# Kernel optimization log

Measured on AMD Instinct MI355X. Metric: run time of the kernel, lower is better.

The kernel has to match this reference:

```python
import jax, jax.numpy as jnp
import numpy as np

B, L = 128, 256
VOCAB, E, PF = 50000, 300, 50
C, K, R = 512, 3, 53
D3 = (E + 2 * PF) * 3  # 1200, conv input channels


def setup_inputs() -> dict:
    key = jax.random.key(0)
    ks = jax.random.split(key, 12)
    return {
        "context": jax.random.randint(ks[0], (B, L), 0, VOCAB),
        "subject_idx": jnp.sort(jax.random.randint(ks[1], (B, 2), 0, L), axis=-1),
        "object_idx": jnp.sort(jax.random.randint(ks[2], (B, 2), 0, L), axis=-1),
        "subject_dis": jax.random.randint(ks[3], (B, L), 0, 2 * L),
        "object_dis": jax.random.randint(ks[4], (B, L), 0, 2 * L),
        "embed_table": jax.random.normal(ks[5], (VOCAB, E), dtype=jnp.float32),
        "pos_table": jax.random.normal(ks[6], (2 * L, PF), dtype=jnp.float32),
        "conv_w": jax.random.normal(ks[7], (C, D3, K), dtype=jnp.float32) * (1.0 / np.sqrt(D3 * K)),
        "conv_b": jax.random.normal(ks[8], (C,), dtype=jnp.float32) * 0.01,
        "rela_linear_w": jax.random.normal(ks[9], (R, C), dtype=jnp.float32) * (1.0 / np.sqrt(C)),
        "rela_emb": jax.random.normal(ks[10], (R, C), dtype=jnp.float32),
    }


def _span_mean(wf3, idx):
    # mean of wf3[b, start:end+1, :] per sample, vectorized with a mask
    pos = jnp.arange(wf3.shape[1])[None, :]
    m = ((pos >= idx[:, 0:1]) & (pos <= idx[:, 1:2])).astype(wf3.dtype)  # B,L
    return jnp.einsum("bld,bl->bd", wf3, m) / jnp.sum(m, axis=1, keepdims=True)


def reference(context, subject_idx, object_idx, subject_dis, object_dis,
              embed_table, pos_table, conv_w, conv_b, rela_linear_w, rela_emb):
    emb = embed_table[context]                                            # B,L,E
    posf = jnp.concatenate([pos_table[subject_dis], pos_table[object_dis]], axis=2)
    wf = jnp.concatenate([emb, posf], axis=2)                             # B,L,D
    wp = jnp.pad(wf, ((0, 0), (1, 1), (0, 0)))
    # sliding window concat of [i-1, i, i+1]
    wf3 = jnp.concatenate([wp[:, :-2], wp[:, 1:-1], wp[:, 2:]], axis=2)   # B,L,3D

    subj = _span_mean(wf3, subject_idx)                                   # B,3D
    obj = _span_mean(wf3, object_idx)
    rs = jax.nn.softmax(jnp.einsum("bld,bd->bl", wf3, subj), axis=1)
    ro = jax.nn.softmax(jnp.einsum("bld,bd->bl", wf3, obj), axis=1)
    wf3 = wf3 * ((rs + ro) * 0.5)[:, :, None]

    x = jnp.transpose(wf3, (0, 2, 1))                                     # B,3D,L
    y = jax.lax.conv_general_dilated(x, conv_w, (1,), [(K // 2, K // 2)],
                                     dimension_numbers=("NCH", "OIH", "NCH"))
    sent = jnp.transpose(jnp.tanh(y + conv_b[None, :, None]), (0, 2, 1))  # B,L,C

    attn = jnp.einsum("blr,rc->blc",
                      jnp.einsum("blc,rc->blr", sent, rela_linear_w), rela_emb)
    attn = jax.nn.softmax(attn, axis=1)  # softmax over sequence positions
    wo = jnp.max(sent * attn, axis=1)                                     # B,C
    wo = wo / jnp.maximum(jnp.linalg.norm(wo, axis=1, keepdims=True), 1e-12)
    all_dist = jnp.linalg.norm(wo[:, None, :] - rela_emb[None, :, :], axis=2)  # B,R
    return all_dist
```

## Files before the change

kernel.cpp:

```cpp
#include <hip/hip_runtime.h>
#include <hip/hip_bf16.h>
#include <math.h>

#define B_  128
#define L_  256
#define E_  300
#define PF_ 50
#define D_  400
#define D3_ 1200
#define C_  512
#define KW_ 3
#define R_  53
#define M_  (B_*L_)
#define KP_ 1216
#define K3_ (3*KP_)
#define LROWS_ 258

typedef __attribute__((ext_vector_type(8))) short bf16x8;
typedef __attribute__((ext_vector_type(8))) unsigned short u16x8;
typedef __attribute__((ext_vector_type(4))) float f32x4;

__device__ __forceinline__ unsigned short f2bf(float f) {
    union { float f; unsigned u; } x; x.f = f;
    unsigned r = x.u + 0x7FFF + ((x.u >> 16) & 1);
    return (unsigned short)(r >> 16);
}
__device__ __forceinline__ float bf2f(unsigned short u) {
    union { unsigned u; float f; } x; x.u = ((unsigned)u) << 16;
    return x.f;
}

__device__ __forceinline__ void gld16(const void* g, void* l) {
    __builtin_amdgcn_global_load_lds(
        (const __attribute__((address_space(1))) void*)g,
        (__attribute__((address_space(3))) void*)l, 16, 0, 0);
}

__global__ void prep_wpT_kernel(const float* __restrict__ conv_w, unsigned short* __restrict__ WpT) {
    int idx = blockIdx.x * blockDim.x + threadIdx.x;
    if (idx >= C_ * K3_) return;
    int c = idx / K3_, q = idx % K3_;
    int k = q / KP_, ch = q % KP_;
    WpT[idx] = (ch < D3_) ? f2bf(conv_w[c * (D3_ * KW_) + ch * KW_ + k]) : (unsigned short)0;
}

__global__ void prep_mT_kernel(const float* __restrict__ rlw, const float* __restrict__ re,
                               unsigned short* __restrict__ MmatT) {
    int idx = blockIdx.x * blockDim.x + threadIdx.x;
    if (idx >= C_ * C_) return;
    int n = idx / C_, k = idx % C_;
    float acc = 0.f;
    for (int r = 0; r < R_; ++r)
        acc += rlw[r * C_ + k] * re[r * C_ + n];
    MmatT[idx] = f2bf(acc);
}

__global__ void build_wf_kernel(const int* __restrict__ ctx, const int* __restrict__ sdis,
                                const int* __restrict__ odis, const float* __restrict__ emb,
                                const float* __restrict__ pos, float* __restrict__ wf) {
    const int total = M_ * D_;
    for (int idx = blockIdx.x * blockDim.x + threadIdx.x; idx < total;
         idx += gridDim.x * blockDim.x) {
        int d = idx % D_;
        int bt = idx / D_;
        float v;
        if (d < E_)            v = emb[(long)ctx[bt] * E_ + d];
        else if (d < E_ + PF_) v = pos[sdis[bt] * PF_ + (d - E_)];
        else                   v = pos[odis[bt] * PF_ + (d - E_ - PF_)];
        wf[idx] = v;
    }
}

__global__ void prefix_wf_kernel(const float* __restrict__ wf, float* __restrict__ Pref) {
    int idx = blockIdx.x * blockDim.x + threadIdx.x;
    if (idx >= B_ * D_) return;
    int b = idx / D_, d = idx % D_;
    const float* src = wf + (size_t)(b << 8) * D_ + d;
    float* dst = Pref + (size_t)(b << 8) * D_ + d;
    float acc = 0.f;
    for (int t = 0; t < L_; ++t) {
        acc += src[(size_t)t * D_];
        dst[(size_t)t * D_] = acc;
    }
}

__global__ void span_mean_kernel(const float* __restrict__ Pref,
                                 const int* __restrict__ sidx, const int* __restrict__ oidx,
                                 float* __restrict__ SS, float* __restrict__ OS) {
    int idx = blockIdx.x * blockDim.x + threadIdx.x;
    if (idx >= B_ * 3 * D_) return;
    int b = idx / (3 * D_);
    int r = idx % (3 * D_);
    int j = r / D_, d = r % D_;

    {
        int s0 = sidx[b * 2], s1 = sidx[b * 2 + 1];
        float inv = 1.f / (float)(s1 - s0 + 1);
        int lo = s0 + j - 1, hi = s1 + j - 1;
        int loc = lo < 0 ? 0 : lo;
        int hic = hi > (L_ - 1) ? (L_ - 1) : hi;
        float sum = 0.f;
        if (loc <= hic) {
            float a = Pref[((size_t)((b << 8) + hic)) * D_ + d];
            float c = (loc > 0) ? Pref[((size_t)((b << 8) + loc - 1)) * D_ + d] : 0.f;
            sum = a - c;
        }
        SS[((size_t)(b * 3 + j)) * D_ + d] = sum * inv;
    }
    {
        int s0 = oidx[b * 2], s1 = oidx[b * 2 + 1];
        float inv = 1.f / (float)(s1 - s0 + 1);
        int lo = s0 + j - 1, hi = s1 + j - 1;
        int loc = lo < 0 ? 0 : lo;
        int hic = hi > (L_ - 1) ? (L_ - 1) : hi;
        float sum = 0.f;
        if (loc <= hic) {
            float a = Pref[((size_t)((b << 8) + hic)) * D_ + d];
            float c = (loc > 0) ? Pref[((size_t)((b << 8) + loc - 1)) * D_ + d] : 0.f;
            sum = a - c;
        }
        OS[((size_t)(b * 3 + j)) * D_ + d] = sum * inv;
    }
}

__global__ __launch_bounds__(256) void dots_kernel(
    const float* __restrict__ wf, const float* __restrict__ SS, const float* __restrict__ OS,
    float* __restrict__ dsb, float* __restrict__ ddb) {
    const int wave = threadIdx.x >> 6, lane = threadIdx.x & 63;
    const int g = blockIdx.x * 4 + wave;
    const int b = g >> 8, t = g & 255;
    float ds = 0.f, dd = 0.f;
#pragma unroll
    for (int j = 0; j < 3; ++j) {
        int u = t + j - 1;
        if ((unsigned)u < (unsigned)L_) {
            const float4* w  = (const float4*)(wf + ((size_t)((b << 8) + u)) * D_);
            const float4* ss = (const float4*)(SS + ((size_t)(b * 3 + j)) * D_);
            const float4* oo = (const float4*)(OS + ((size_t)(b * 3 + j)) * D_);
            for (int q = lane; q < D_ / 4; q += 64) {
                float4 wv = w[q], sv = ss[q], ov = oo[q];
                ds += wv.x * sv.x + wv.y * sv.y + wv.z * sv.z + wv.w * sv.w;
                dd += wv.x * ov.x + wv.y * ov.y + wv.z * ov.z + wv.w * ov.w;
            }
        }
    }
#pragma unroll
    for (int off = 32; off > 0; off >>= 1) {
        ds += __shfl_down(ds, off);
        dd += __shfl_down(dd, off);
    }
    if (lane == 0) { dsb[g] = ds; ddb[g] = dd; }
}

__global__ __launch_bounds__(256) void softmax_s_kernel(
    const float* __restrict__ dsb, const float* __restrict__ ddb, float* __restrict__ s) {
    const int b = blockIdx.x, tid = threadIdx.x;
    __shared__ float red[256];
    float ds = dsb[(b << 8) + tid];
    float dd = ddb[(b << 8) + tid];

    red[tid] = ds; __syncthreads();
    for (int st = 128; st > 0; st >>= 1) {
        if (tid < st) red[tid] = fmaxf(red[tid], red[tid + st]);
        __syncthreads();
    }
    float ms = red[0]; __syncthreads();
    float es = expf(ds - ms);
    red[tid] = es; __syncthreads();
    for (int st = 128; st > 0; st >>= 1) {
        if (tid < st) red[tid] += red[tid + st];
        __syncthreads();
    }
    float zs = red[0]; __syncthreads();

    red[tid] = dd; __syncthreads();
    for (int st = 128; st > 0; st >>= 1) {
        if (tid < st) red[tid] = fmaxf(red[tid], red[tid + st]);
        __syncthreads();
    }
    float mo = red[0]; __syncthreads();
    float eo = expf(dd - mo);
    red[tid] = eo; __syncthreads();
    for (int st = 128; st > 0; st >>= 1) {
        if (tid < st) red[tid] += red[tid + st];
        __syncthreads();
    }
    float zo = red[0];

    s[(b << 8) + tid] = 0.5f * (es / zs + eo / zo);
}

__global__ void build_xsp_kernel(const float* __restrict__ wf, const float* __restrict__ s,
                                 unsigned short* __restrict__ XSp) {
    const int CH8 = KP_ / 8;
    int idx = blockIdx.x * blockDim.x + threadIdx.x;
    const int total = B_ * LROWS_ * CH8;
    if (idx >= total) return;
    int chunk = idx % CH8;
    int rb = idx / CH8;
    int row = rb % LROWS_;
    int b = rb / LROWS_;

    u16x8 out = {0,0,0,0,0,0,0,0};
    int t = row - 1;
    int ch0 = chunk * 8;
    if ((unsigned)t < (unsigned)L_ && ch0 < D3_) {
        int j = ch0 / D_;
        int d0 = ch0 - j * D_;
        int u = t + j - 1;
        if ((unsigned)u < (unsigned)L_) {
            float sc = s[(b << 8) + t];
            const float* w = wf + ((size_t)((b << 8) + u)) * D_ + d0;
#pragma unroll
            for (int q = 0; q < 8; ++q) out[q] = f2bf(sc * w[q]);
        }
    }
    *(u16x8*)&XSp[((size_t)(b * LROWS_ + row)) * KP_ + ch0] = out;
}

template<int MODE>
__global__ __launch_bounds__(512, 2) void gemm8_kernel(
    const unsigned short* __restrict__ Aglob, const unsigned short* __restrict__ Bglob,
    const float* __restrict__ conv_b, unsigned short* __restrict__ outb,
    float* __restrict__ outf) {
    extern __shared__ unsigned short lds[];
    const int tid = threadIdx.x;
    const int lane = tid & 63;
    const int wave = tid >> 6;
    const int wr = wave >> 2;
    const int wc = wave & 3;
    const int bx = blockIdx.x;
    const int blockN = blockIdx.y * 256;
    const int l15 = lane & 15;
    const int NT = (MODE == 0) ? (K3_ / 64) : (C_ / 64);
    const size_t Astr = (MODE == 0) ? (size_t)KP_ : (size_t)C_;
    const size_t Bstr = (MODE == 0) ? (size_t)K3_ : (size_t)C_;

    const int arole = wc;
    const int bhalf = wc >> 1;
    const int brole = wr * 2 + (wc & 1);

    const int acol0 = (((lane >> 4) + 0) ^ (l15 & 7)) * 8;
    const int acol1 = (((lane >> 4) + 4) ^ (l15 & 7)) * 8;
    const int bro = (wc & 1) * 64;

    auto stageA = [&](int kt, int buf) {
        const unsigned short* gb;
        if constexpr (MODE == 0) {
            int tap = kt / KP_, ch0 = kt - tap * KP_;
            gb = Aglob + ((size_t)(bx * LROWS_ + wr * 128 + tap)) * KP_ + ch0;
        } else {
            gb = Aglob + ((size_t)(bx * 256 + wr * 128)) * C_ + kt;
        }
        unsigned short* pb = &lds[(buf * 2 + wr) * 8192];
#pragma unroll
        for (int i = 0; i < 4; ++i) {
            int sl = arole * 256 + i * 64 + lane;
            int row = sl >> 3, p = sl & 7;
            int colg = p ^ (row & 7);
            gld16(gb + (size_t)row * Astr + colg * 8, (char*)pb + sl * 16);
        }
    };
    auto stageB = [&](int kt, int buf) {
        const unsigned short* gb = Bglob + ((size_t)(blockN + bhalf * 128)) * Bstr + kt;
        unsigned short* pb = &lds[32768 + (buf * 2 + bhalf) * 8192];
#pragma unroll
        for (int i = 0; i < 4; ++i) {
            int sl = brole * 256 + i * 64 + lane;
            int row = sl >> 3, p = sl & 7;
            int colg = p ^ (row & 7);
            gld16(gb + (size_t)row * Bstr + colg * 8, (char*)pb + sl * 16);
        }
    };

    f32x4 acc[8][4] = {};

    stageA(0, 0);
    stageB(0, 0);
    __syncthreads();

    int cur = 0;
    for (int kt = 0; kt < NT * 64; kt += 64, cur ^= 1) {
        int ktn = kt + 64;
        if (ktn >= NT * 64) ktn = 0;
        const unsigned short* Ap = &lds[(cur * 2 + wr) * 8192];
        const unsigned short* Bp = &lds[32768 + (cur * 2 + bhalf) * 8192];

        bf16x8 a[8], b0, b1;

#pragma unroll
        for (int mi = 0; mi < 8; ++mi) a[mi] = *(const bf16x8*)&Ap[(mi * 16 + l15) * 64 + acol0];
        b0 = *(const bf16x8*)&Bp[(bro + 0 * 16 + l15) * 64 + acol0];
        b1 = *(const bf16x8*)&Bp[(bro + 1 * 16 + l15) * 64 + acol0];
        stageA(ktn, cur ^ 1);
        __builtin_amdgcn_s_setprio(1);
#pragma unroll
        for (int mi = 0; mi < 8; ++mi) {
            acc[mi][0] = __builtin_amdgcn_mfma_f32_16x16x32_bf16(a[mi], b0, acc[mi][0], 0, 0, 0);
            acc[mi][1] = __builtin_amdgcn_mfma_f32_16x16x32_bf16(a[mi], b1, acc[mi][1], 0, 0, 0);
        }
        __builtin_amdgcn_s_setprio(0);

        b0 = *(const bf16x8*)&Bp[(bro + 2 * 16 + l15) * 64 + acol0];
        b1 = *(const bf16x8*)&Bp[(bro + 3 * 16 + l15) * 64 + acol0];
        stageB(ktn, cur ^ 1);
        __builtin_amdgcn_s_setprio(1);
#pragma unroll
        for (int mi = 0; mi < 8; ++mi) {
            acc[mi][2] = __builtin_amdgcn_mfma_f32_16x16x32_bf16(a[mi], b0, acc[mi][2], 0, 0, 0);
            acc[mi][3] = __builtin_amdgcn_mfma_f32_16x16x32_bf16(a[mi], b1, acc[mi][3], 0, 0, 0);
        }
        __builtin_amdgcn_s_setprio(0);

#pragma unroll
        for (int mi = 0; mi < 8; ++mi) a[mi] = *(const bf16x8*)&Ap[(mi * 16 + l15) * 64 + acol1];
        b0 = *(const bf16x8*)&Bp[(bro + 0 * 16 + l15) * 64 + acol1];
        b1 = *(const bf16x8*)&Bp[(bro + 1 * 16 + l15) * 64 + acol1];
        __builtin_amdgcn_s_setprio(1);
#pragma unroll
        for (int mi = 0; mi < 8; ++mi) {
            acc[mi][0] = __builtin_amdgcn_mfma_f32_16x16x32_bf16(a[mi], b0, acc[mi][0], 0, 0, 0);
            acc[mi][1] = __builtin_amdgcn_mfma_f32_16x16x32_bf16(a[mi], b1, acc[mi][1], 0, 0, 0);
        }
        __builtin_amdgcn_s_setprio(0);

        b0 = *(const bf16x8*)&Bp[(bro + 2 * 16 + l15) * 64 + acol1];
        b1 = *(const bf16x8*)&Bp[(bro + 3 * 16 + l15) * 64 + acol1];
        __builtin_amdgcn_s_setprio(1);
#pragma unroll
        for (int mi = 0; mi < 8; ++mi) {
            acc[mi][2] = __builtin_amdgcn_mfma_f32_16x16x32_bf16(a[mi], b0, acc[mi][2], 0, 0, 0);
            acc[mi][3] = __builtin_amdgcn_mfma_f32_16x16x32_bf16(a[mi], b1, acc[mi][3], 0, 0, 0);
        }
        __builtin_amdgcn_s_setprio(0);

        __syncthreads();
    }

    const int r4 = ((lane >> 4) << 2);
#pragma unroll
    for (int mi = 0; mi < 8; ++mi) {
#pragma unroll
        for (int nj = 0; nj < 4; ++nj) {
            const int col = blockN + wc * 64 + nj * 16 + l15;
            const int row0 = bx * 256 + wr * 128 + mi * 16 + r4;
            if constexpr (MODE == 0) {
                float bias = conv_b[col];
#pragma unroll
                for (int r = 0; r < 4; ++r)
                    outb[(size_t)(row0 + r) * C_ + col] = f2bf(tanhf(acc[mi][nj][r] + bias));
            } else {
#pragma unroll
                for (int r = 0; r < 4; ++r)
                    outf[(size_t)(row0 + r) * C_ + col] = acc[mi][nj][r];
            }
        }
    }
}

__global__ __launch_bounds__(256) void softmax_wo_kernel(
    const float* __restrict__ P, const unsigned short* __restrict__ sent,
    float* __restrict__ wo) {
    const int b = blockIdx.x;
    const int c = blockIdx.y * 256 + threadIdx.x;
    const float* Pb = P + ((size_t)(b << 8)) * C_ + c;
    const unsigned short* Sb = sent + ((size_t)(b << 8)) * C_ + c;
    float m = -INFINITY;
    for (int l = 0; l < L_; ++l) m = fmaxf(m, Pb[(size_t)l * C_]);
    float z = 0.f, wmax = -INFINITY;
    for (int l = 0; l < L_; ++l) {
        float e = expf(Pb[(size_t)l * C_] - m);
        z += e;
        wmax = fmaxf(wmax, bf2f(Sb[(size_t)l * C_]) * e);
    }
    wo[b * C_ + c] = wmax / z;
}

__global__ __launch_bounds__(256) void final_kernel(
    const float* __restrict__ wo, const float* __restrict__ re, float* __restrict__ out) {
    const int b = blockIdx.x, tid = threadIdx.x;
    __shared__ float won[C_];
    __shared__ float red[256];
    float p = 0.f;
    for (int c = tid; c < C_; c += 256) {
        float v = wo[b * C_ + c];
        p += v * v;
    }
    red[tid] = p; __syncthreads();
    for (int st = 128; st > 0; st >>= 1) {
        if (tid < st) red[tid] += red[tid + st];
        __syncthreads();
    }
    float inv = 1.f / fmaxf(sqrtf(red[0]), 1e-12f);
    for (int c = tid; c < C_; c += 256) won[c] = wo[b * C_ + c] * inv;
    __syncthreads();
    const int wv = tid >> 6, lane = tid & 63;
    for (int r = wv; r < R_; r += 4) {
        float acc2 = 0.f;
        for (int c = lane; c < C_; c += 64) {
            float dlt = won[c] - re[r * C_ + c];
            acc2 += dlt * dlt;
        }
        for (int off = 32; off > 0; off >>= 1) acc2 += __shfl_down(acc2, off);
        if (lane == 0) out[b * R_ + r] = sqrtf(acc2);
    }
}

extern "C" void kernel_launch(void* const* d_in, const int* in_sizes, int n_in,
                              void* d_out, int out_size, void* d_ws, size_t ws_size,
                              hipStream_t stream) {
    const int* context     = (const int*)d_in[0];
    const int* subject_idx = (const int*)d_in[1];
    const int* object_idx  = (const int*)d_in[2];
    const int* subject_dis = (const int*)d_in[3];
    const int* object_dis  = (const int*)d_in[4];
    const float* embed_table = (const float*)d_in[5];
    const float* pos_table   = (const float*)d_in[6];
    const float* conv_w      = (const float*)d_in[7];
    const float* conv_b      = (const float*)d_in[8];
    const float* rlw         = (const float*)d_in[9];
    const float* re          = (const float*)d_in[10];
    float* out = (float*)d_out;

    char* ws = (char*)d_ws;
    size_t off = 0;
    auto alloc = [&](size_t bytes) {
        void* p = ws + off;
        off = (off + bytes + 255) & ~(size_t)255;
        return p;
    };
    float* wf            = (float*)alloc((size_t)M_ * D_ * 4);
    float* s             = (float*)alloc((size_t)M_ * 4);
    unsigned short* XSp  = (unsigned short*)alloc((size_t)B_ * LROWS_ * KP_ * 2);
    unsigned short* WpT  = (unsigned short*)alloc((size_t)C_ * K3_ * 2);
    unsigned short* MmatT= (unsigned short*)alloc((size_t)C_ * C_ * 2);
    unsigned short* sent = (unsigned short*)alloc((size_t)M_ * C_ * 2);
    float* wo            = (float*)alloc((size_t)B_ * C_ * 4);
    float* SS            = (float*)alloc((size_t)B_ * 3 * D_ * 4);
    float* OS            = (float*)alloc((size_t)B_ * 3 * D_ * 4);
    float* dsb           = (float*)alloc((size_t)M_ * 4);
    float* ddb           = (float*)alloc((size_t)M_ * 4);
    float* Pref = (float*)XSp;
    float* P    = (float*)XSp;

    (void)hipFuncSetAttribute((const void*)gemm8_kernel<0>,
                              hipFuncAttributeMaxDynamicSharedMemorySize, 131072);
    (void)hipFuncSetAttribute((const void*)gemm8_kernel<1>,
                              hipFuncAttributeMaxDynamicSharedMemorySize, 131072);

    prep_wpT_kernel<<<(C_ * K3_ + 255) / 256, 256, 0, stream>>>(conv_w, WpT);
    prep_mT_kernel<<<(C_ * C_ + 255) / 256, 256, 0, stream>>>(rlw, re, MmatT);
    build_wf_kernel<<<4096, 256, 0, stream>>>(context, subject_dis, object_dis,
                                              embed_table, pos_table, wf);
    prefix_wf_kernel<<<(B_ * D_ + 255) / 256, 256, 0, stream>>>(wf, Pref);
    span_mean_kernel<<<(B_ * 3 * D_ + 255) / 256, 256, 0, stream>>>(Pref, subject_idx,
                                                                    object_idx, SS, OS);
    dots_kernel<<<M_ / 4, 256, 0, stream>>>(wf, SS, OS, dsb, ddb);
    softmax_s_kernel<<<B_, 256, 0, stream>>>(dsb, ddb, s);
    build_xsp_kernel<<<(B_ * LROWS_ * (KP_ / 8) + 255) / 256, 256, 0, stream>>>(wf, s, XSp);
    gemm8_kernel<0><<<dim3(M_ / 256, C_ / 256), 512, 131072, stream>>>(
        XSp, WpT, conv_b, sent, nullptr);
    gemm8_kernel<1><<<dim3(M_ / 256, C_ / 256), 512, 131072, stream>>>(
        sent, MmatT, nullptr, nullptr, P);
    softmax_wo_kernel<<<dim3(B_, 2), 256, 0, stream>>>(P, sent, wo);
    final_kernel<<<B_, 256, 0, stream>>>(wo, re, out);
}
```

Before: 315.0 us.

## Split conv GEMM into smaller-tile kernel and fuse softmax-max into P GEMM

Replaces the shared 256x256-tile GEMM template with a dedicated conv kernel that uses 128x128 tiles, 4 waves, and a swizzled block order. This raises the block count from 256 to 1024 to improve CU occupancy and L2 locality. The second GEMM now also performs the per-column softmax/max reduction itself, after a block sync, which removes a separate kernel launch. The fused epilogue uses only half the threads and re-reads P from global memory, so that tail stays serial.

```diff
diff --git a/kernel.cpp b/kernel.cpp
--- a/kernel.cpp
+++ b/kernel.cpp
@@ -218,11 +218,95 @@
     *(u16x8*)&XSp[((size_t)(b * LROWS_ + row)) * KP_ + ch0] = out;
 }
 
-template<int MODE>
-__global__ __launch_bounds__(512, 2) void gemm8_kernel(
-    const unsigned short* __restrict__ Aglob, const unsigned short* __restrict__ Bglob,
-    const float* __restrict__ conv_b, unsigned short* __restrict__ outb,
-    float* __restrict__ outf) {
+__global__ __launch_bounds__(256) void conv4_kernel(
+    const unsigned short* __restrict__ XSp, const unsigned short* __restrict__ WpT,
+    const float* __restrict__ conv_b, unsigned short* __restrict__ sent) {
+    extern __shared__ unsigned short lds[];
+    const int tid = threadIdx.x;
+    const int lane = tid & 63;
+    const int wave = tid >> 6;
+    const int wr = wave >> 1, wc = wave & 1;
+    const int lin = blockIdx.y * 256 + blockIdx.x;
+    const int swz = (lin & 7) * 128 + (lin >> 3);
+    const int bx = swz & 255;
+    const int by = swz >> 8;
+    const int l15 = lane & 15;
+    const int acol0 = (((lane >> 4) + 0) ^ (l15 & 7)) * 8;
+    const int acol1 = (((lane >> 4) + 4) ^ (l15 & 7)) * 8;
+    const int NT = K3_ / 64;
+
+    const int xrow0 = (bx >> 1) * LROWS_ + (bx & 1) * 128;
+
+    auto stage = [&](int kt, int buf) {
+        int tap = kt / KP_, ch0 = kt - tap * KP_;
+        const unsigned short* ga = XSp + ((size_t)(xrow0 + tap)) * KP_ + ch0;
+        const unsigned short* gb = WpT + ((size_t)(by * 128)) * K3_ + kt;
+        unsigned short* pa = &lds[buf * 8192];
+        unsigned short* pb = &lds[16384 + buf * 8192];
+#pragma unroll
+        for (int i = 0; i < 4; ++i) {
+            int sl = i * 256 + tid;
+            int row = sl >> 3, p = sl & 7;
+            int colg = p ^ (row & 7);
+            gld16(ga + (size_t)row * KP_ + colg * 8, (char*)pa + sl * 16);
+            gld16(gb + (size_t)row * K3_ + colg * 8, (char*)pb + sl * 16);
+        }
+    };
+
+    f32x4 acc[4][4] = {};
+
+    stage(0, 0);
+    __syncthreads();
+
+    int cur = 0;
+    for (int kt = 0; kt < NT * 64; kt += 64, cur ^= 1) {
+        int ktn = kt + 64;
+        if (ktn >= NT * 64) ktn = 0;
+        const unsigned short* Ap = &lds[cur * 8192];
+        const unsigned short* Bp = &lds[16384 + cur * 8192];
+
+        bf16x8 a0[4], b0[4], a1[4], b1[4];
+#pragma unroll
+        for (int i = 0; i < 4; ++i) {
+            a0[i] = *(const bf16x8*)&Ap[(wr * 64 + i * 16 + l15) * 64 + acol0];
+            b0[i] = *(const bf16x8*)&Bp[(wc * 64 + i * 16 + l15) * 64 + acol0];
+            a1[i] = *(const bf16x8*)&Ap[(wr * 64 + i * 16 + l15) * 64 + acol1];
+            b1[i] = *(const bf16x8*)&Bp[(wc * 64 + i * 16 + l15) * 64 + acol1];
+        }
+        stage(ktn, cur ^ 1);
+        __builtin_amdgcn_s_setprio(1);
+#pragma unroll
+        for (int i = 0; i < 4; ++i)
+#pragma unroll
+            for (int j = 0; j < 4; ++j)
+                acc[i][j] = __builtin_amdgcn_mfma_f32_16x16x32_bf16(a0[i], b0[j], acc[i][j], 0, 0, 0);
+#pragma unroll
+        for (int i = 0; i < 4; ++i)
+#pragma unroll
+            for (int j = 0; j < 4; ++j)
+                acc[i][j] = __builtin_amdgcn_mfma_f32_16x16x32_bf16(a1[i], b1[j], acc[i][j], 0, 0, 0);
+        __builtin_amdgcn_s_setprio(0);
+        __syncthreads();
+    }
+
+    const int r4 = ((lane >> 4) << 2);
+#pragma unroll
+    for (int mi = 0; mi < 4; ++mi) {
+#pragma unroll
+        for (int nj = 0; nj < 4; ++nj) {
+            const int col = by * 128 + wc * 64 + nj * 16 + l15;
+            const int row0 = bx * 128 + wr * 64 + mi * 16 + r4;
+            float bias = conv_b[col];
+#pragma unroll
+            for (int r = 0; r < 4; ++r)
+                sent[(size_t)(row0 + r) * C_ + col] = f2bf(tanhf(acc[mi][nj][r] + bias));
+        }
+    }
+}
+
+__global__ __launch_bounds__(512) void pgemm_kernel(
+    const unsigned short* __restrict__ sent, const unsigned short* __restrict__ MmatT,
+    float* __restrict__ P, float* __restrict__ wo) {
     extern __shared__ unsigned short lds[];
     const int tid = threadIdx.x;
     const int lane = tid & 63;
@@ -232,9 +316,7 @@
     const int bx = blockIdx.x;
     const int blockN = blockIdx.y * 256;
     const int l15 = lane & 15;
-    const int NT = (MODE == 0) ? (K3_ / 64) : (C_ / 64);
-    const size_t Astr = (MODE == 0) ? (size_t)KP_ : (size_t)C_;
-    const size_t Bstr = (MODE == 0) ? (size_t)K3_ : (size_t)C_;
+    const int NT = C_ / 64;
 
     const int arole = wc;
     const int bhalf = wc >> 1;
@@ -245,31 +327,25 @@
     const int bro = (wc & 1) * 64;
 
     auto stageA = [&](int kt, int buf) {
-        const unsigned short* gb;
-        if constexpr (MODE == 0) {
-            int tap = kt / KP_, ch0 = kt - tap * KP_;
-            gb = Aglob + ((size_t)(bx * LROWS_ + wr * 128 + tap)) * KP_ + ch0;
-        } else {
-            gb = Aglob + ((size_t)(bx * 256 + wr * 128)) * C_ + kt;
-        }
+        const unsigned short* gb = sent + ((size_t)(bx * 256 + wr * 128)) * C_ + kt;
         unsigned short* pb = &lds[(buf * 2 + wr) * 8192];
 #pragma unroll
         for (int i = 0; i < 4; ++i) {
             int sl = arole * 256 + i * 64 + lane;
             int row = sl >> 3, p = sl & 7;
             int colg = p ^ (row & 7);
-            gld16(gb + (size_t)row * Astr + colg * 8, (char*)pb + sl * 16);
+            gld16(gb + (size_t)row * C_ + colg * 8, (char*)pb + sl * 16);
         }
     };
     auto stageB = [&](int kt, int buf) {
-        const unsigned short* gb = Bglob + ((size_t)(blockN + bhalf * 128)) * Bstr + kt;
+        const unsigned short* gb = MmatT + ((size_t)(blockN + bhalf * 128)) * C_ + kt;
         unsigned short* pb = &lds[32768 + (buf * 2 + bhalf) * 8192];
 #pragma unroll
         for (int i = 0; i < 4; ++i) {
             int sl = brole * 256 + i * 64 + lane;
             int row = sl >> 3, p = sl & 7;
             int colg = p ^ (row & 7);
-            gld16(gb + (size_t)row * Bstr + colg * 8, (char*)pb + sl * 16);
+            gld16(gb + (size_t)row * C_ + colg * 8, (char*)pb + sl * 16);
         }
     };
 
@@ -344,36 +420,28 @@
         for (int nj = 0; nj < 4; ++nj) {
             const int col = blockN + wc * 64 + nj * 16 + l15;
             const int row0 = bx * 256 + wr * 128 + mi * 16 + r4;
-            if constexpr (MODE == 0) {
-                float bias = conv_b[col];
-#pragma unroll
-                for (int r = 0; r < 4; ++r)
-                    outb[(size_t)(row0 + r) * C_ + col] = f2bf(tanhf(acc[mi][nj][r] + bias));
-            } else {
-#pragma unroll
-                for (int r = 0; r < 4; ++r)
-                    outf[(size_t)(row0 + r) * C_ + col] = acc[mi][nj][r];
-            }
-        }
-    }
-}
-
-__global__ __launch_bounds__(256) void softmax_wo_kernel(
-    const float* __restrict__ P, const unsigned short* __restrict__ sent,
-    float* __restrict__ wo) {
-    const int b = blockIdx.x;
-    const int c = blockIdx.y * 256 + threadIdx.x;
-    const float* Pb = P + ((size_t)(b << 8)) * C_ + c;
-    const unsigned short* Sb = sent + ((size_t)(b << 8)) * C_ + c;
-    float m = -INFINITY;
-    for (int l = 0; l < L_; ++l) m = fmaxf(m, Pb[(size_t)l * C_]);
-    float z = 0.f, wmax = -INFINITY;
-    for (int l = 0; l < L_; ++l) {
-        float e = expf(Pb[(size_t)l * C_] - m);
-        z += e;
-        wmax = fmaxf(wmax, bf2f(Sb[(size_t)l * C_]) * e);
-    }
-    wo[b * C_ + c] = wmax / z;
+#pragma unroll
+            for (int r = 0; r < 4; ++r)
+                P[(size_t)(row0 + r) * C_ + col] = acc[mi][nj][r];
+        }
+    }
+
+    __syncthreads();
+
+    if (tid < 256) {
+        const int col = blockN + tid;
+        const float* Pb = P + ((size_t)(bx * 256)) * C_ + col;
+        const unsigned short* Sb = sent + ((size_t)(bx * 256)) * C_ + col;
+        float m = -INFINITY;
+        for (int l = 0; l < L_; ++l) m = fmaxf(m, Pb[(size_t)l * C_]);
+        float z = 0.f, wmax = -INFINITY;
+        for (int l = 0; l < L_; ++l) {
+            float e = expf(Pb[(size_t)l * C_] - m);
+            z += e;
+            wmax = fmaxf(wmax, bf2f(Sb[(size_t)l * C_]) * e);
+        }
+        wo[bx * C_ + col] = wmax / z;
+    }
 }
 
 __global__ __launch_bounds__(256) void final_kernel(
@@ -443,9 +511,9 @@
     float* Pref = (float*)XSp;
     float* P    = (float*)XSp;
 
-    (void)hipFuncSetAttribute((const void*)gemm8_kernel<0>,
-                              hipFuncAttributeMaxDynamicSharedMemorySize, 131072);
-    (void)hipFuncSetAttribute((const void*)gemm8_kernel<1>,
+    (void)hipFuncSetAttribute((const void*)conv4_kernel,
+                              hipFuncAttributeMaxDynamicSharedMemorySize, 65536);
+    (void)hipFuncSetAttribute((const void*)pgemm_kernel,
                               hipFuncAttributeMaxDynamicSharedMemorySize, 131072);
 
     prep_wpT_kernel<<<(C_ * K3_ + 255) / 256, 256, 0, stream>>>(conv_w, WpT);
@@ -458,10 +526,7 @@
     dots_kernel<<<M_ / 4, 256, 0, stream>>>(wf, SS, OS, dsb, ddb);
     softmax_s_kernel<<<B_, 256, 0, stream>>>(dsb, ddb, s);
     build_xsp_kernel<<<(B_ * LROWS_ * (KP_ / 8) + 255) / 256, 256, 0, stream>>>(wf, s, XSp);
-    gemm8_kernel<0><<<dim3(M_ / 256, C_ / 256), 512, 131072, stream>>>(
-        XSp, WpT, conv_b, sent, nullptr);
-    gemm8_kernel<1><<<dim3(M_ / 256, C_ / 256), 512, 131072, stream>>>(
-        sent, MmatT, nullptr, nullptr, P);
-    softmax_wo_kernel<<<dim3(B_, 2), 256, 0, stream>>>(P, sent, wo);
+    conv4_kernel<<<dim3(256, 4), 256, 65536, stream>>>(XSp, WpT, conv_b, sent);
+    pgemm_kernel<<<dim3(M_ / 256, C_ / 256), 512, 131072, stream>>>(sent, MmatT, P, wo);
     final_kernel<<<B_, 256, 0, stream>>>(wo, re, out);
 }
```

After: 352.0 us. 1.12x slower.

## Fuse span-mean, attention dots and softmax into one per-batch kernel

Applied to the files above, without the earlier changes.

Replaces the prefix-sum, span-mean, dot-product and softmax kernels with one kernel per batch sample. The subject and object span means are accumulated directly with masked column sums into shared memory, then reused for the per-position dots. The softmax runs in the same block. This removes the large prefix buffer write and read-back, the intermediate buffers and three launches. In exchange the fused stage runs only 128 blocks, which may underuse the GPU for the column scans and dot products.

```diff
diff --git a/kernel.cpp b/kernel.cpp
--- a/kernel.cpp
+++ b/kernel.cpp
@@ -71,123 +71,97 @@
     }
 }
 
-__global__ void prefix_wf_kernel(const float* __restrict__ wf, float* __restrict__ Pref) {
-    int idx = blockIdx.x * blockDim.x + threadIdx.x;
-    if (idx >= B_ * D_) return;
-    int b = idx / D_, d = idx % D_;
-    const float* src = wf + (size_t)(b << 8) * D_ + d;
-    float* dst = Pref + (size_t)(b << 8) * D_ + d;
-    float acc = 0.f;
-    for (int t = 0; t < L_; ++t) {
-        acc += src[(size_t)t * D_];
-        dst[(size_t)t * D_] = acc;
-    }
-}
-
-__global__ void span_mean_kernel(const float* __restrict__ Pref,
-                                 const int* __restrict__ sidx, const int* __restrict__ oidx,
-                                 float* __restrict__ SS, float* __restrict__ OS) {
-    int idx = blockIdx.x * blockDim.x + threadIdx.x;
-    if (idx >= B_ * 3 * D_) return;
-    int b = idx / (3 * D_);
-    int r = idx % (3 * D_);
-    int j = r / D_, d = r % D_;
-
-    {
-        int s0 = sidx[b * 2], s1 = sidx[b * 2 + 1];
-        float inv = 1.f / (float)(s1 - s0 + 1);
-        int lo = s0 + j - 1, hi = s1 + j - 1;
-        int loc = lo < 0 ? 0 : lo;
-        int hic = hi > (L_ - 1) ? (L_ - 1) : hi;
-        float sum = 0.f;
-        if (loc <= hic) {
-            float a = Pref[((size_t)((b << 8) + hic)) * D_ + d];
-            float c = (loc > 0) ? Pref[((size_t)((b << 8) + loc - 1)) * D_ + d] : 0.f;
-            sum = a - c;
-        }
-        SS[((size_t)(b * 3 + j)) * D_ + d] = sum * inv;
-    }
-    {
-        int s0 = oidx[b * 2], s1 = oidx[b * 2 + 1];
-        float inv = 1.f / (float)(s1 - s0 + 1);
-        int lo = s0 + j - 1, hi = s1 + j - 1;
-        int loc = lo < 0 ? 0 : lo;
-        int hic = hi > (L_ - 1) ? (L_ - 1) : hi;
-        float sum = 0.f;
-        if (loc <= hic) {
-            float a = Pref[((size_t)((b << 8) + hic)) * D_ + d];
-            float c = (loc > 0) ? Pref[((size_t)((b << 8) + loc - 1)) * D_ + d] : 0.f;
-            sum = a - c;
-        }
-        OS[((size_t)(b * 3 + j)) * D_ + d] = sum * inv;
-    }
-}
-
-__global__ __launch_bounds__(256) void dots_kernel(
-    const float* __restrict__ wf, const float* __restrict__ SS, const float* __restrict__ OS,
-    float* __restrict__ dsb, float* __restrict__ ddb) {
-    const int wave = threadIdx.x >> 6, lane = threadIdx.x & 63;
-    const int g = blockIdx.x * 4 + wave;
-    const int b = g >> 8, t = g & 255;
-    float ds = 0.f, dd = 0.f;
-#pragma unroll
-    for (int j = 0; j < 3; ++j) {
-        int u = t + j - 1;
-        if ((unsigned)u < (unsigned)L_) {
-            const float4* w  = (const float4*)(wf + ((size_t)((b << 8) + u)) * D_);
-            const float4* ss = (const float4*)(SS + ((size_t)(b * 3 + j)) * D_);
-            const float4* oo = (const float4*)(OS + ((size_t)(b * 3 + j)) * D_);
-            for (int q = lane; q < D_ / 4; q += 64) {
-                float4 wv = w[q], sv = ss[q], ov = oo[q];
-                ds += wv.x * sv.x + wv.y * sv.y + wv.z * sv.z + wv.w * sv.w;
-                dd += wv.x * ov.x + wv.y * ov.y + wv.z * ov.z + wv.w * ov.w;
+__global__ __launch_bounds__(512) void attn_fused_kernel(
+    const float* __restrict__ wf, const int* __restrict__ sidx, const int* __restrict__ oidx,
+    float* __restrict__ s) {
+    const int b = blockIdx.x;
+    const int tid = threadIdx.x;
+    __shared__ float subjS[3][D_];
+    __shared__ float objS[3][D_];
+    __shared__ float dbuf[2][L_];
+    __shared__ float red[512];
+
+    const int s0 = sidx[b * 2], s1 = sidx[b * 2 + 1];
+    const int o0 = oidx[b * 2], o1 = oidx[b * 2 + 1];
+    const float sinv = 1.0f / (float)(s1 - s0 + 1);
+    const float oinv = 1.0f / (float)(o1 - o0 + 1);
+
+    if (tid < D_) {
+        float ss0 = 0.f, ss1 = 0.f, ss2 = 0.f, oo0 = 0.f, oo1 = 0.f, oo2 = 0.f;
+        const float* col = wf + (size_t)(b << 8) * D_ + tid;
+        for (int t = 0; t < L_; ++t) {
+            float v = col[(size_t)t * D_];
+            int t1 = t + 1;
+            if (t1 - 0 >= s0 && t1 - 0 <= s1) ss0 += v;
+            if (t1 - 1 >= s0 && t1 - 1 <= s1) ss1 += v;
+            if (t1 - 2 >= s0 && t1 - 2 <= s1) ss2 += v;
+            if (t1 - 0 >= o0 && t1 - 0 <= o1) oo0 += v;
+            if (t1 - 1 >= o0 && t1 - 1 <= o1) oo1 += v;
+            if (t1 - 2 >= o0 && t1 - 2 <= o1) oo2 += v;
+        }
+        subjS[0][tid] = ss0 * sinv; subjS[1][tid] = ss1 * sinv; subjS[2][tid] = ss2 * sinv;
+        objS[0][tid] = oo0 * oinv;  objS[1][tid] = oo1 * oinv;  objS[2][tid] = oo2 * oinv;
+    }
+    __syncthreads();
+
+    const int wv = tid >> 6, lane = tid & 63;
+    for (int t = wv; t < L_; t += 8) {
+        float ds = 0.f, dd = 0.f;
+#pragma unroll
+        for (int j = 0; j < 3; ++j) {
+            int u = t + j - 1;
+            if ((unsigned)u < (unsigned)L_) {
+                const float4* w4 = (const float4*)(wf + ((size_t)((b << 8) + u)) * D_);
+                const float4* s4 = (const float4*)&subjS[j][0];
+                const float4* o4 = (const float4*)&objS[j][0];
+                for (int q = lane; q < D_ / 4; q += 64) {
+                    float4 wv4 = w4[q], sv = s4[q], ov = o4[q];
+                    ds += wv4.x * sv.x + wv4.y * sv.y + wv4.z * sv.z + wv4.w * sv.w;
+                    dd += wv4.x * ov.x + wv4.y * ov.y + wv4.z * ov.z + wv4.w * ov.w;
+                }
             }
         }
-    }
-#pragma unroll
-    for (int off = 32; off > 0; off >>= 1) {
-        ds += __shfl_down(ds, off);
-        dd += __shfl_down(dd, off);
-    }
-    if (lane == 0) { dsb[g] = ds; ddb[g] = dd; }
-}
-
-__global__ __launch_bounds__(256) void softmax_s_kernel(
-    const float* __restrict__ dsb, const float* __restrict__ ddb, float* __restrict__ s) {
-    const int b = blockIdx.x, tid = threadIdx.x;
-    __shared__ float red[256];
-    float ds = dsb[(b << 8) + tid];
-    float dd = ddb[(b << 8) + tid];
+#pragma unroll
+        for (int off = 32; off > 0; off >>= 1) {
+            ds += __shfl_down(ds, off);
+            dd += __shfl_down(dd, off);
+        }
+        if (lane == 0) { dbuf[0][t] = ds; dbuf[1][t] = dd; }
+    }
+    __syncthreads();
+
+    float ds = (tid < L_) ? dbuf[0][tid] : -INFINITY;
+    float dd = (tid < L_) ? dbuf[1][tid] : -INFINITY;
 
     red[tid] = ds; __syncthreads();
-    for (int st = 128; st > 0; st >>= 1) {
+    for (int st = 256; st > 0; st >>= 1) {
         if (tid < st) red[tid] = fmaxf(red[tid], red[tid + st]);
         __syncthreads();
     }
     float ms = red[0]; __syncthreads();
-    float es = expf(ds - ms);
+    float es = (tid < L_) ? expf(ds - ms) : 0.f;
     red[tid] = es; __syncthreads();
-    for (int st = 128; st > 0; st >>= 1) {
+    for (int st = 256; st > 0; st >>= 1) {
         if (tid < st) red[tid] += red[tid + st];
         __syncthreads();
     }
     float zs = red[0]; __syncthreads();
 
     red[tid] = dd; __syncthreads();
-    for (int st = 128; st > 0; st >>= 1) {
+    for (int st = 256; st > 0; st >>= 1) {
         if (tid < st) red[tid] = fmaxf(red[tid], red[tid + st]);
         __syncthreads();
     }
     float mo = red[0]; __syncthreads();
-    float eo = expf(dd - mo);
+    float eo = (tid < L_) ? expf(dd - mo) : 0.f;
     red[tid] = eo; __syncthreads();
-    for (int st = 128; st > 0; st >>= 1) {
+    for (int st = 256; st > 0; st >>= 1) {
         if (tid < st) red[tid] += red[tid + st];
         __syncthreads();
     }
     float zo = red[0];
 
-    s[(b << 8) + tid] = 0.5f * (es / zs + eo / zo);
+    if (tid < L_) s[(b << 8) + tid] = 0.5f * (es / zs + eo / zo);
 }
 
 __global__ void build_xsp_kernel(const float* __restrict__ wf, const float* __restrict__ s,
@@ -436,12 +410,7 @@
     unsigned short* MmatT= (unsigned short*)alloc((size_t)C_ * C_ * 2);
     unsigned short* sent = (unsigned short*)alloc((size_t)M_ * C_ * 2);
     float* wo            = (float*)alloc((size_t)B_ * C_ * 4);
-    float* SS            = (float*)alloc((size_t)B_ * 3 * D_ * 4);
-    float* OS            = (float*)alloc((size_t)B_ * 3 * D_ * 4);
-    float* dsb           = (float*)alloc((size_t)M_ * 4);
-    float* ddb           = (float*)alloc((size_t)M_ * 4);
-    float* Pref = (float*)XSp;
-    float* P    = (float*)XSp;
+    float* P = (float*)XSp;
 
     (void)hipFuncSetAttribute((const void*)gemm8_kernel<0>,
                               hipFuncAttributeMaxDynamicSharedMemorySize, 131072);
@@ -452,11 +421,7 @@
     prep_mT_kernel<<<(C_ * C_ + 255) / 256, 256, 0, stream>>>(rlw, re, MmatT);
     build_wf_kernel<<<4096, 256, 0, stream>>>(context, subject_dis, object_dis,
                                               embed_table, pos_table, wf);
-    prefix_wf_kernel<<<(B_ * D_ + 255) / 256, 256, 0, stream>>>(wf, Pref);
-    span_mean_kernel<<<(B_ * 3 * D_ + 255) / 256, 256, 0, stream>>>(Pref, subject_idx,
-                                                                    object_idx, SS, OS);
-    dots_kernel<<<M_ / 4, 256, 0, stream>>>(wf, SS, OS, dsb, ddb);
-    softmax_s_kernel<<<B_, 256, 0, stream>>>(dsb, ddb, s);
+    attn_fused_kernel<<<B_, 512, 0, stream>>>(wf, subject_idx, object_idx, s);
     build_xsp_kernel<<<(B_ * LROWS_ * (KP_ / 8) + 255) / 256, 256, 0, stream>>>(wf, s, XSp);
     gemm8_kernel<0><<<dim3(M_ / 256, C_ / 256), 512, 131072, stream>>>(
         XSp, WpT, conv_b, sent, nullptr);
```

Measured after the change: 391.5 us. +24.3%, slower.
